# Kernel tuning notes

Measured on AMD Instinct MI355X. Metric: run time of the kernel, lower is better.

Reference implementation:

```python
import jax, jax.numpy as jnp
import numpy as np

QUALITY_ALPHA = 1.0
TOPK = 4
MIX_BETA = 0.5
NEG = -1e9


def setup_inputs() -> dict:
    key = jax.random.key(0)
    ks = jax.random.split(key, 12)
    B, S, D, H, Q, QH = 64, 2048, 512, 128, 4, 32
    feats = jax.random.normal(ks[0], (B, S, D), dtype=jnp.float32)
    mask = jax.random.uniform(ks[1], (B, S)) > 0.3
    mask = mask.at[:, 0].set(True)  # guarantee >=1 valid segment per row
    seg_quality = jax.random.normal(ks[2], (B, S, Q), dtype=jnp.float32)
    W1 = jax.random.normal(ks[3], (D, H), dtype=jnp.float32) * 0.05
    b1 = jnp.zeros((H,), dtype=jnp.float32)
    w2 = jax.random.normal(ks[4], (H, 1), dtype=jnp.float32) * 0.05
    b2 = jnp.zeros((1,), dtype=jnp.float32)
    qW1 = jax.random.normal(ks[5], (Q, QH), dtype=jnp.float32) * 0.05
    qb1 = jnp.zeros((QH,), dtype=jnp.float32)
    qw2 = jax.random.normal(ks[6], (QH, 1), dtype=jnp.float32) * 0.05
    qb2 = jnp.zeros((1,), dtype=jnp.float32)
    return dict(feats=feats, mask=mask, seg_quality=seg_quality,
                W1=W1, b1=b1, w2=w2, b2=b2, qW1=qW1, qb1=qb1, qw2=qw2, qb2=qb2)


def _masked_softmax(logits, mask):
    logits = jnp.where(mask, logits, NEG)
    w = jax.nn.softmax(logits, axis=1)
    w = w * mask.astype(w.dtype)
    return w / jnp.maximum(w.sum(axis=1, keepdims=True), 1e-8)


def reference(feats, mask, seg_quality, W1, b1, w2, b2, qW1, qb1, qw2, qb2):
    # evidence scorer: Linear -> tanh -> Linear  ([B,S,D] -> [B,S])
    evidence = (jnp.tanh(jnp.einsum('bsd,dh->bsh', feats, W1) + b1) @ w2)[..., 0] + b2[0]
    # quality net: Linear -> relu -> Linear  ([B,S,Q] -> [B,S])
    quality = (jax.nn.relu(jnp.einsum('bsq,qh->bsh', seg_quality, qW1) + qb1) @ qw2)[..., 0] + qb2[0]
    combined = evidence + QUALITY_ALPHA * quality

    weights = _masked_softmax(combined, mask)
    attn_pooled = jnp.einsum('bsd,bs->bd', feats, weights)

    # top-k path on combined logits
    masked_scores = jnp.where(mask, combined, NEG)
    _, topk_indices = jax.lax.top_k(masked_scores, TOPK)          # [B, k]
    topk_feats = jnp.take_along_axis(feats, topk_indices[..., None], axis=1)  # [B, k, D]
    topk_valid = jnp.take_along_axis(mask, topk_indices, axis=1)  # [B, k] bool
    denom = jnp.maximum(topk_valid.astype(feats.dtype).sum(axis=1, keepdims=True), 1.0)
    topk_pooled = (topk_feats * topk_valid[..., None].astype(feats.dtype)).sum(axis=1) / denom

    pooled = MIX_BETA * attn_pooled + (1.0 - MIX_BETA) * topk_pooled
    return pooled, weights, attn_pooled, topk_pooled, topk_indices, topk_valid
```

## Files before the change

kernel.cpp:

```cpp
#include <hip/hip_runtime.h>
#include <cstdint>
#include <cstddef>

#define B 64
#define S 2048
#define D 512
#define H 128
#define Q 4
#define QH 32
#define KTOP 4
#define NROWS (B * S)
#define NEGV -1e9f
#define NCH 32
#define SC (S / NCH)
#define ZPB (S / 128)

typedef __bf16 bf16x8 __attribute__((ext_vector_type(8)));
typedef float f32x4 __attribute__((ext_vector_type(4)));
typedef unsigned short us8 __attribute__((ext_vector_type(8)));

__device__ __forceinline__ unsigned hasbyte(unsigned v, unsigned c) {
    unsigned x = v ^ (c * 0x01010101u);
    return (x - 0x01010101u) & ~x & 0x80808080u;
}

__device__ __forceinline__ void split_f32(float x, unsigned short& hi, unsigned short& lo) {
    unsigned bx = __float_as_uint(x);
    hi = (unsigned short)(bx >> 16);
    float fh = __uint_as_float(bx & 0xFFFF0000u);
    lo = (unsigned short)(__float_as_uint(x - fh) >> 16);
}

__device__ __forceinline__ float tanh_f(float x) {
    float e = __expf(2.f * x);
    return 1.f - __fdividef(2.f, e + 1.f);
}

__device__ __forceinline__ void gll16(const void* g, void* l) {
    __builtin_amdgcn_global_load_lds(
        (const __attribute__((address_space(1))) unsigned int*)g,
        (__attribute__((address_space(3))) unsigned int*)l, 16, 0, 0);
}

__global__ __launch_bounds__(256) void prep_kernel(
    const float* __restrict__ W1, unsigned short* __restrict__ bh,
    unsigned short* __restrict__ bl, const unsigned char* __restrict__ m,
    int* __restrict__ mode, const float* __restrict__ segq,
    const float* __restrict__ qW1, const float* __restrict__ qb1,
    const float* __restrict__ qw2, const float* __restrict__ qb2,
    float* __restrict__ qual) {
    const int t = threadIdx.x;
    const int bid = blockIdx.x;
    if (bid < 256) {
        int i = bid * 256 + t;
        int h = i >> 9, k = i & 511;
        float x = W1[(size_t)k * H + h];
        unsigned short hv, lv;
        split_f32(x, hv, lv);
        bh[i] = hv;
        bl[i] = lv;
        return;
    }
    if (bid == 256) {
        __shared__ int fF0, fF, fB, fO4;
        if (t == 0) { fF0 = 0; fF = 0; fB = 0; fO4 = 0; }
        __syncthreads();
        const uint4* mv = (const uint4*)m;
        int a = 0, bb = 0, c = 0, d = 0;
        for (int i = t; i < NROWS / 16; i += 256) {
            uint4 v = mv[i];
            if (hasbyte(v.x, 0xF0u) | hasbyte(v.y, 0xF0u) | hasbyte(v.z, 0xF0u) | hasbyte(v.w, 0xF0u)) a = 1;
            if (hasbyte(v.x, 0x3Fu) | hasbyte(v.y, 0x3Fu) | hasbyte(v.z, 0x3Fu) | hasbyte(v.w, 0x3Fu) |
                hasbyte(v.x, 0x80u) | hasbyte(v.y, 0x80u) | hasbyte(v.z, 0x80u) | hasbyte(v.w, 0x80u)) bb = 1;
            if ((v.x & 0xFFFFFF00u) | (v.y & 0xFFFFFF00u) | (v.z & 0xFFFFFF00u) | (v.w & 0xFFFFFF00u)) c = 1;
            if ((v.y & 0xFFu) | (v.w & 0xFFu)) d = 1;
        }
        if (a) atomicOr(&fF0, 1);
        if (bb) atomicOr(&fF, 1);
        if (c) atomicOr(&fB, 1);
        if (d) atomicOr(&fO4, 1);
        __syncthreads();
        if (t == 0) {
            int md;
            if (fF0) md = 4;
            else if (fF) md = 3;
            else if (fB) md = 0;
            else if (fO4) md = 1;
            else md = 2;
            *mode = md;
        }
        return;
    }
    __shared__ float sW[Q * QH];
    __shared__ float sb1[QH];
    __shared__ float sw2[QH];
    __shared__ float sb2v;
    if (t < Q * QH) sW[t] = qW1[t];
    if (t >= 128 && t < 128 + QH) sb1[t - 128] = qb1[t - 128];
    if (t >= 160 && t < 160 + QH) sw2[t - 160] = qw2[t - 160];
    if (t == 192) sb2v = qb2[0];
    __syncthreads();
    const int i = (bid - 257) * 256 + t;
    float4 sq = *reinterpret_cast<const float4*>(&segq[(size_t)i * Q]);
    float s = 0.f;
#pragma unroll
    for (int h = 0; h < QH; ++h) {
        float a = sq.x * sW[h] + sq.y * sW[QH + h] + sq.z * sW[2 * QH + h] + sq.w * sW[3 * QH + h] + sb1[h];
        a = fmaxf(a, 0.f);
        s += a * sw2[h];
    }
    qual[i] = s + sb2v;
}

__global__ __launch_bounds__(256) void evidence_mfma_kernel(
    const float* __restrict__ feats, const unsigned short* __restrict__ wbh,
    const unsigned short* __restrict__ wbl, const float* __restrict__ b1g,
    const float* __restrict__ w2g, const float* __restrict__ b2g,
    const float* __restrict__ qual, const void* __restrict__ mraw,
    const int* __restrict__ mode, float* __restrict__ comb,
    float* __restrict__ ew, float* __restrict__ Zpart) {
    __shared__ unsigned short sAh[128][32];
    __shared__ unsigned short sAl[128][32];
    __shared__ unsigned short sBh[128][32];
    __shared__ unsigned short sBl[128][32];
    __shared__ float red[128][2];
    __shared__ float sew[128];

    const int t = threadIdx.x;
    const int lane = t & 63;
    const int wid = t >> 6;
    const int wm = wid >> 1, wn = wid & 1;
    const int l16 = lane & 15, lk = lane >> 4;
    const int row0 = blockIdx.x * 128;
    const int md = *mode;

    f32x4 acc[4][4];
#pragma unroll
    for (int mf = 0; mf < 4; ++mf)
#pragma unroll
        for (int nf = 0; nf < 4; ++nf) acc[mf][nf] = (f32x4)0.f;

    const int ar = t >> 1;
    const int akh = (t & 1) * 16;
    const float* fsrc = feats + (size_t)(row0 + ar) * D + akh;

    const int e0 = ((wid * 2 + 0) * 64 + lane) * 8;
    const int e1 = ((wid * 2 + 1) * 64 + lane) * 8;
    const int h0b = e0 >> 5, k0b = e0 & 31;
    const int h1b = e1 >> 5, k1b = e1 & 31;
    char* sBh0 = (char*)&sBh[0][0] + (wid * 2 + 0) * 1024;
    char* sBh1 = (char*)&sBh[0][0] + (wid * 2 + 1) * 1024;
    char* sBl0 = (char*)&sBl[0][0] + (wid * 2 + 0) * 1024;
    char* sBl1 = (char*)&sBl[0][0] + (wid * 2 + 1) * 1024;

    for (int kc = 0; kc < D; kc += 32) {
        gll16(wbh + (size_t)h0b * D + kc + k0b, sBh0);
        gll16(wbh + (size_t)h1b * D + kc + k1b, sBh1);
        gll16(wbl + (size_t)h0b * D + kc + k0b, sBl0);
        gll16(wbl + (size_t)h1b * D + kc + k1b, sBl1);

        float f[16];
        *reinterpret_cast<float4*>(&f[0]) = *reinterpret_cast<const float4*>(fsrc + kc + 0);
        *reinterpret_cast<float4*>(&f[4]) = *reinterpret_cast<const float4*>(fsrc + kc + 4);
        *reinterpret_cast<float4*>(&f[8]) = *reinterpret_cast<const float4*>(fsrc + kc + 8);
        *reinterpret_cast<float4*>(&f[12]) = *reinterpret_cast<const float4*>(fsrc + kc + 12);
        us8 vh0, vh1, vl0, vl1;
#pragma unroll
        for (int j = 0; j < 8; ++j) {
            unsigned short hh, ll;
            split_f32(f[j], hh, ll);
            vh0[j] = hh; vl0[j] = ll;
        }
#pragma unroll
        for (int j = 0; j < 8; ++j) {
            unsigned short hh, ll;
            split_f32(f[8 + j], hh, ll);
            vh1[j] = hh; vl1[j] = ll;
        }
        *reinterpret_cast<us8*>(&sAh[ar][akh]) = vh0;
        *reinterpret_cast<us8*>(&sAh[ar][akh + 8]) = vh1;
        *reinterpret_cast<us8*>(&sAl[ar][akh]) = vl0;
        *reinterpret_cast<us8*>(&sAl[ar][akh + 8]) = vl1;

        __syncthreads();

        bf16x8 ah[4], al[4], bh[4], bl[4];
#pragma unroll
        for (int mf = 0; mf < 4; ++mf) {
            int rr = wm * 64 + mf * 16 + l16;
            ah[mf] = *reinterpret_cast<const bf16x8*>(&sAh[rr][lk * 8]);
            al[mf] = *reinterpret_cast<const bf16x8*>(&sAl[rr][lk * 8]);
        }
#pragma unroll
        for (int nf = 0; nf < 4; ++nf) {
            int hh = wn * 64 + nf * 16 + l16;
            bh[nf] = *reinterpret_cast<const bf16x8*>(&sBh[hh][lk * 8]);
            bl[nf] = *reinterpret_cast<const bf16x8*>(&sBl[hh][lk * 8]);
        }
#pragma unroll
        for (int mf = 0; mf < 4; ++mf)
#pragma unroll
            for (int nf = 0; nf < 4; ++nf) {
                acc[mf][nf] = __builtin_amdgcn_mfma_f32_16x16x32_bf16(ah[mf], bh[nf], acc[mf][nf], 0, 0, 0);
                acc[mf][nf] = __builtin_amdgcn_mfma_f32_16x16x32_bf16(ah[mf], bl[nf], acc[mf][nf], 0, 0, 0);
                acc[mf][nf] = __builtin_amdgcn_mfma_f32_16x16x32_bf16(al[mf], bh[nf], acc[mf][nf], 0, 0, 0);
            }
        __syncthreads();
    }

    float b1v[4], w2v[4];
#pragma unroll
    for (int nf = 0; nf < 4; ++nf) {
        int hh = wn * 64 + nf * 16 + l16;
        b1v[nf] = b1g[hh];
        w2v[nf] = w2g[hh];
    }
    float rs[4][4];
#pragma unroll
    for (int mf = 0; mf < 4; ++mf)
#pragma unroll
        for (int r2 = 0; r2 < 4; ++r2) {
            float s = 0.f;
#pragma unroll
            for (int nf = 0; nf < 4; ++nf) s += tanh_f(acc[mf][nf][r2] + b1v[nf]) * w2v[nf];
            s += __shfl_xor(s, 1, 16);
            s += __shfl_xor(s, 2, 16);
            s += __shfl_xor(s, 4, 16);
            s += __shfl_xor(s, 8, 16);
            rs[mf][r2] = s;
        }
    if (l16 == 0) {
#pragma unroll
        for (int mf = 0; mf < 4; ++mf)
#pragma unroll
            for (int r2 = 0; r2 < 4; ++r2) red[wm * 64 + mf * 16 + lk * 4 + r2][wn] = rs[mf][r2];
    }
    __syncthreads();

    if (t < 128) {
        const int row = row0 + t;
        float mv;
        switch (md) {
            case 0: mv = ((const unsigned char*)mraw)[row] ? 1.f : 0.f; break;
            case 1: mv = ((const int*)mraw)[row] ? 1.f : 0.f; break;
            case 2: mv = ((const long long*)mraw)[row] ? 1.f : 0.f; break;
            case 3: mv = (((const float*)mraw)[row] != 0.f) ? 1.f : 0.f; break;
            default: mv = (((const double*)mraw)[row] != 0.0) ? 1.f : 0.f; break;
        }
        float e = red[t][0] + red[t][1] + b2g[0];
        float c = (mv != 0.f) ? (e + qual[row]) : NEGV;
        comb[row] = c;
        float x = __expf(c);
        ew[row] = x;
        sew[t] = x;
    }
    __syncthreads();
    if (t < 64) {
        float z = sew[t] + sew[t + 64];
#pragma unroll
        for (int o = 32; o > 0; o >>= 1) z += __shfl_xor(z, o, 64);
        if (t == 0) Zpart[blockIdx.x] = z;
    }
}

__global__ __launch_bounds__(256) void pool_partial_kernel(
    const float* __restrict__ feats, const float* __restrict__ ew, float* __restrict__ part) {
    const int b = blockIdx.y, ch = blockIdx.x, t = threadIdx.x;
    const int s0 = ch * SC;
    __shared__ float sw[SC];
    __shared__ float4 redp[256];
    if (t < SC) sw[t] = ew[(size_t)b * S + s0 + t];
    __syncthreads();
    const int dq = (t & 127) * 4;
    const int rp = t >> 7;
    float4 a = {0.f, 0.f, 0.f, 0.f};
    const float* fp = feats + ((size_t)b * S + s0 + rp) * D + dq;
    for (int s = rp; s < SC; s += 2) {
        float wv = sw[s];
        if (wv != 0.f) {
            float4 f = *reinterpret_cast<const float4*>(fp);
            a.x += wv * f.x; a.y += wv * f.y; a.z += wv * f.z; a.w += wv * f.w;
        }
        fp += 2 * D;
    }
    redp[t] = a;
    __syncthreads();
    if (t < 128) {
        float4 o = redp[t], o2 = redp[t + 128];
        o.x += o2.x; o.y += o2.y; o.z += o2.z; o.w += o2.w;
        *reinterpret_cast<float4*>(&part[((size_t)(b * NCH + ch)) * D + dq]) = o;
    }
}

__global__ __launch_bounds__(256) void finalize_kernel(
    const float* __restrict__ comb, const float* __restrict__ Zpart,
    const float* __restrict__ part, const float* __restrict__ feats,
    float* __restrict__ o_weights, float* __restrict__ o_tidx, float* __restrict__ o_tval,
    float* __restrict__ o_attn, float* __restrict__ o_topk, float* __restrict__ o_pooled) {
    __shared__ float sinv;
    __shared__ float mvv[256 * 4];
    __shared__ int mii[256 * 4];
    __shared__ int sti[4];
    __shared__ float stv[4];
    __shared__ float sdn;
    const int b = blockIdx.x, t = threadIdx.x;
    const float* row = comb + (size_t)b * S;

    if (t == 0) {
        float z = 0.f;
#pragma unroll
        for (int j = 0; j < ZPB; ++j) z += Zpart[b * ZPB + j];
        sinv = 1.f / fmaxf(z, 1e-8f);
    }
    __syncthreads();
    const float inv = sinv;

    float tv[4] = {-3e38f, -3e38f, -3e38f, -3e38f};
    int ti[4] = {1 << 30, 1 << 30, 1 << 30, 1 << 30};
    for (int s = t; s < S; s += 256) {
        float v = row[s];
        o_weights[(size_t)b * S + s] = __expf(v) * inv;
        if (v > tv[3]) {
            tv[3] = v; ti[3] = s;
#pragma unroll
            for (int k = 3; k > 0; --k) {
                bool up = (tv[k] > tv[k - 1]) || (tv[k] == tv[k - 1] && ti[k] < ti[k - 1]);
                if (up) {
                    float fv = tv[k]; tv[k] = tv[k - 1]; tv[k - 1] = fv;
                    int ii = ti[k]; ti[k] = ti[k - 1]; ti[k - 1] = ii;
                }
            }
        }
    }
#pragma unroll
    for (int k = 0; k < 4; ++k) { mvv[t * 4 + k] = tv[k]; mii[t * 4 + k] = ti[k]; }
    __syncthreads();
    for (int st = 128; st >= 1; st >>= 1) {
        if (t < st) {
            float av[4], bv[4];
            int ai[4], bi[4];
#pragma unroll
            for (int k = 0; k < 4; ++k) {
                av[k] = mvv[t * 4 + k]; ai[k] = mii[t * 4 + k];
                bv[k] = mvv[(t + st) * 4 + k]; bi[k] = mii[(t + st) * 4 + k];
            }
            float rv[4]; int ri[4];
            int i = 0, j = 0;
            for (int o = 0; o < 4; ++o) {
                bool ta = (av[i] > bv[j]) || (av[i] == bv[j] && ai[i] < bi[j]);
                if (ta) { rv[o] = av[i]; ri[o] = ai[i]; ++i; }
                else { rv[o] = bv[j]; ri[o] = bi[j]; ++j; }
            }
#pragma unroll
            for (int k = 0; k < 4; ++k) { mvv[t * 4 + k] = rv[k]; mii[t * 4 + k] = ri[k]; }
        }
        __syncthreads();
    }
    if (t == 0) {
        float dn = 0.f;
#pragma unroll
        for (int k = 0; k < 4; ++k) {
            int idx = mii[k];
            int valid = (mvv[k] > -1e8f) ? 1 : 0;
            sti[k] = idx;
            stv[k] = (float)valid;
            o_tidx[b * 4 + k] = (float)idx;
            o_tval[b * 4 + k] = (float)valid;
            dn += (float)valid;
        }
        sdn = fmaxf(dn, 1.f);
    }
    __syncthreads();

    const int i0 = sti[0], i1 = sti[1], i2 = sti[2], i3 = sti[3];
    const float v0 = stv[0], v1 = stv[1], v2 = stv[2], v3 = stv[3];
    const float inv_dn = 1.f / sdn;
    for (int d = t; d < D; d += 256) {
        float s = 0.f;
#pragma unroll
        for (int ch = 0; ch < NCH; ++ch) s += part[((size_t)(b * NCH + ch)) * D + d];
        s *= inv;
        float tk = v0 * feats[((size_t)b * S + i0) * D + d] + v1 * feats[((size_t)b * S + i1) * D + d] +
                   v2 * feats[((size_t)b * S + i2) * D + d] + v3 * feats[((size_t)b * S + i3) * D + d];
        tk *= inv_dn;
        o_attn[(size_t)b * D + d] = s;
        o_topk[(size_t)b * D + d] = tk;
        o_pooled[(size_t)b * D + d] = 0.5f * s + 0.5f * tk;
    }
}

extern "C" void kernel_launch(void* const* d_in, const int* in_sizes, int n_in,
                              void* d_out, int out_size, void* d_ws, size_t ws_size,
                              hipStream_t stream) {
    const float* feats = (const float*)d_in[0];
    const void* maskraw = d_in[1];
    const float* segq = (const float*)d_in[2];
    const float* W1 = (const float*)d_in[3];
    const float* b1 = (const float*)d_in[4];
    const float* w2 = (const float*)d_in[5];
    const float* b2 = (const float*)d_in[6];
    const float* qW1 = (const float*)d_in[7];
    const float* qb1 = (const float*)d_in[8];
    const float* qw2 = (const float*)d_in[9];
    const float* qb2 = (const float*)d_in[10];

    char* ws = (char*)d_ws;
    int* mode = (int*)ws;
    float* comb = (float*)(ws + 16);
    float* ewb = comb + NROWS;
    float* qual = ewb + NROWS;
    float* part = qual + NROWS;
    float* Zpart = part + (size_t)B * NCH * D;
    unsigned short* wsBh = (unsigned short*)(Zpart + 1024);
    unsigned short* wsBl = wsBh + (size_t)H * D;

    float* out = (float*)d_out;
    float* o_pooled = out;
    float* o_weights = out + (size_t)B * D;
    float* o_attn = o_weights + (size_t)B * S;
    float* o_topk = o_attn + (size_t)B * D;
    float* o_tidx = o_topk + (size_t)B * D;
    float* o_tval = o_tidx + (size_t)B * KTOP;

    prep_kernel<<<257 + NROWS / 256, 256, 0, stream>>>(
        W1, wsBh, wsBl, (const unsigned char*)maskraw, mode,
        segq, qW1, qb1, qw2, qb2, qual);
    evidence_mfma_kernel<<<NROWS / 128, 256, 0, stream>>>(
        feats, wsBh, wsBl, b1, w2, b2, qual, maskraw, mode, comb, ewb, Zpart);
    pool_partial_kernel<<<dim3(NCH, B), 256, 0, stream>>>(feats, ewb, part);
    finalize_kernel<<<B, 256, 0, stream>>>(comb, Zpart, part, feats, o_weights,
                                           o_tidx, o_tval, o_attn, o_topk, o_pooled);
}
```

Measured before the change: 134.3 us.

## Halve evidence GEMM row tile and reverse pool block order for L2 reuse

Changes the evidence MFMA kernel to process 64 rows per block instead of 128, which doubles the block count and shrinks per-thread accumulators. The intent is better occupancy and more blocks in flight. The cost is reloading the W1 hi/lo tiles twice as often. The pool_partial kernel now walks batches and chunks in reverse so it first touches the feats rows the evidence kernel wrote most recently, which are likely still resident in L2/LLC.

Measured after the change: 148.1 us. 1.1x slower.

```diff
diff --git a/kernel.cpp b/kernel.cpp
--- a/kernel.cpp
+++ b/kernel.cpp
@@ -13,7 +13,9 @@
 #define NEGV -1e9f
 #define NCH 32
 #define SC (S / NCH)
-#define ZPB (S / 128)
+#define EROWS 64
+#define NEBLK (NROWS / EROWS)
+#define ZPB (S / EROWS)
 
 typedef __bf16 bf16x8 __attribute__((ext_vector_type(8)));
 typedef float f32x4 __attribute__((ext_vector_type(4)));
@@ -119,30 +121,30 @@
     const float* __restrict__ qual, const void* __restrict__ mraw,
     const int* __restrict__ mode, float* __restrict__ comb,
     float* __restrict__ ew, float* __restrict__ Zpart) {
-    __shared__ unsigned short sAh[128][32];
-    __shared__ unsigned short sAl[128][32];
+    __shared__ unsigned short sAh[EROWS][32];
+    __shared__ unsigned short sAl[EROWS][32];
     __shared__ unsigned short sBh[128][32];
     __shared__ unsigned short sBl[128][32];
-    __shared__ float red[128][2];
-    __shared__ float sew[128];
+    __shared__ float red[EROWS][2];
+    __shared__ float sew[EROWS];
 
     const int t = threadIdx.x;
     const int lane = t & 63;
     const int wid = t >> 6;
     const int wm = wid >> 1, wn = wid & 1;
     const int l16 = lane & 15, lk = lane >> 4;
-    const int row0 = blockIdx.x * 128;
+    const int row0 = blockIdx.x * EROWS;
     const int md = *mode;
 
-    f32x4 acc[4][4];
-#pragma unroll
-    for (int mf = 0; mf < 4; ++mf)
+    f32x4 acc[2][4];
+#pragma unroll
+    for (int mf = 0; mf < 2; ++mf)
 #pragma unroll
         for (int nf = 0; nf < 4; ++nf) acc[mf][nf] = (f32x4)0.f;
 
-    const int ar = t >> 1;
-    const int akh = (t & 1) * 16;
-    const float* fsrc = feats + (size_t)(row0 + ar) * D + akh;
+    const int ar = t >> 2;
+    const int ao = (t & 3) * 8;
+    const float* fsrc = feats + (size_t)(row0 + ar) * D + ao;
 
     const int e0 = ((wid * 2 + 0) * 64 + lane) * 8;
     const int e1 = ((wid * 2 + 1) * 64 + lane) * 8;
@@ -159,35 +161,25 @@
         gll16(wbl + (size_t)h0b * D + kc + k0b, sBl0);
         gll16(wbl + (size_t)h1b * D + kc + k1b, sBl1);
 
-        float f[16];
+        float f[8];
         *reinterpret_cast<float4*>(&f[0]) = *reinterpret_cast<const float4*>(fsrc + kc + 0);
         *reinterpret_cast<float4*>(&f[4]) = *reinterpret_cast<const float4*>(fsrc + kc + 4);
-        *reinterpret_cast<float4*>(&f[8]) = *reinterpret_cast<const float4*>(fsrc + kc + 8);
-        *reinterpret_cast<float4*>(&f[12]) = *reinterpret_cast<const float4*>(fsrc + kc + 12);
-        us8 vh0, vh1, vl0, vl1;
+        us8 vh, vl;
 #pragma unroll
         for (int j = 0; j < 8; ++j) {
             unsigned short hh, ll;
             split_f32(f[j], hh, ll);
-            vh0[j] = hh; vl0[j] = ll;
-        }
-#pragma unroll
-        for (int j = 0; j < 8; ++j) {
-            unsigned short hh, ll;
-            split_f32(f[8 + j], hh, ll);
-            vh1[j] = hh; vl1[j] = ll;
-        }
-        *reinterpret_cast<us8*>(&sAh[ar][akh]) = vh0;
-        *reinterpret_cast<us8*>(&sAh[ar][akh + 8]) = vh1;
-        *reinterpret_cast<us8*>(&sAl[ar][akh]) = vl0;
-        *reinterpret_cast<us8*>(&sAl[ar][akh + 8]) = vl1;
+            vh[j] = hh; vl[j] = ll;
+        }
+        *reinterpret_cast<us8*>(&sAh[ar][ao]) = vh;
+        *reinterpret_cast<us8*>(&sAl[ar][ao]) = vl;
 
         __syncthreads();
 
-        bf16x8 ah[4], al[4], bh[4], bl[4];
-#pragma unroll
-        for (int mf = 0; mf < 4; ++mf) {
-            int rr = wm * 64 + mf * 16 + l16;
+        bf16x8 ah[2], al[2], bh[4], bl[4];
+#pragma unroll
+        for (int mf = 0; mf < 2; ++mf) {
+            int rr = wm * 32 + mf * 16 + l16;
             ah[mf] = *reinterpret_cast<const bf16x8*>(&sAh[rr][lk * 8]);
             al[mf] = *reinterpret_cast<const bf16x8*>(&sAl[rr][lk * 8]);
         }
@@ -198,7 +190,7 @@
             bl[nf] = *reinterpret_cast<const bf16x8*>(&sBl[hh][lk * 8]);
         }
 #pragma unroll
-        for (int mf = 0; mf < 4; ++mf)
+        for (int mf = 0; mf < 2; ++mf)
 #pragma unroll
             for (int nf = 0; nf < 4; ++nf) {
                 acc[mf][nf] = __builtin_amdgcn_mfma_f32_16x16x32_bf16(ah[mf], bh[nf], acc[mf][nf], 0, 0, 0);
@@ -215,9 +207,8 @@
         b1v[nf] = b1g[hh];
         w2v[nf] = w2g[hh];
     }
-    float rs[4][4];
-#pragma unroll
-    for (int mf = 0; mf < 4; ++mf)
+#pragma unroll
+    for (int mf = 0; mf < 2; ++mf)
 #pragma unroll
         for (int r2 = 0; r2 < 4; ++r2) {
             float s = 0.f;
@@ -227,17 +218,11 @@
             s += __shfl_xor(s, 2, 16);
             s += __shfl_xor(s, 4, 16);
             s += __shfl_xor(s, 8, 16);
-            rs[mf][r2] = s;
-        }
-    if (l16 == 0) {
-#pragma unroll
-        for (int mf = 0; mf < 4; ++mf)
-#pragma unroll
-            for (int r2 = 0; r2 < 4; ++r2) red[wm * 64 + mf * 16 + lk * 4 + r2][wn] = rs[mf][r2];
-    }
-    __syncthreads();
-
-    if (t < 128) {
+            if (l16 == 0) red[wm * 32 + mf * 16 + lk * 4 + r2][wn] = s;
+        }
+    __syncthreads();
+
+    if (t < EROWS) {
         const int row = row0 + t;
         float mv;
         switch (md) {
@@ -256,7 +241,7 @@
     }
     __syncthreads();
     if (t < 64) {
-        float z = sew[t] + sew[t + 64];
+        float z = sew[t];
 #pragma unroll
         for (int o = 32; o > 0; o >>= 1) z += __shfl_xor(z, o, 64);
         if (t == 0) Zpart[blockIdx.x] = z;
@@ -265,7 +250,9 @@
 
 __global__ __launch_bounds__(256) void pool_partial_kernel(
     const float* __restrict__ feats, const float* __restrict__ ew, float* __restrict__ part) {
-    const int b = blockIdx.y, ch = blockIdx.x, t = threadIdx.x;
+    const int ch = (NCH - 1) - blockIdx.x;
+    const int b = (B - 1) - blockIdx.y;
+    const int t = threadIdx.x;
     const int s0 = ch * SC;
     __shared__ float sw[SC];
     __shared__ float4 redp[256];
@@ -411,7 +398,7 @@
     float* qual = ewb + NROWS;
     float* part = qual + NROWS;
     float* Zpart = part + (size_t)B * NCH * D;
-    unsigned short* wsBh = (unsigned short*)(Zpart + 1024);
+    unsigned short* wsBh = (unsigned short*)(Zpart + NEBLK);
     unsigned short* wsBl = wsBh + (size_t)H * D;
 
     float* out = (float*)d_out;
@@ -425,7 +412,7 @@
     prep_kernel<<<257 + NROWS / 256, 256, 0, stream>>>(
         W1, wsBh, wsBl, (const unsigned char*)maskraw, mode,
         segq, qW1, qb1, qw2, qb2, qual);
-    evidence_mfma_kernel<<<NROWS / 128, 256, 0, stream>>>(
+    evidence_mfma_kernel<<<NEBLK, 256, 0, stream>>>(
         feats, wsBh, wsBl, b1, w2, b2, qual, maskraw, mode, comb, ewb, Zpart);
     pool_partial_kernel<<<dim3(NCH, B), 256, 0, stream>>>(feats, ewb, part);
     finalize_kernel<<<B, 256, 0, stream>>>(comb, Zpart, part, feats, o_weights,
```
